# Kernel tuning notes

Hardware: AMD Instinct MI355X
Metric: run time of the kernel (lower is better)

## Reference

```python
import jax, jax.numpy as jnp
import numpy as np


def _lc2d(x, W, b, kh, kw):
    """Locally connected conv: distinct (Cout,Cin,kh,kw) kernel per output location.
    x: [B,Cin,H,W]; W: [Hout,Wout,Cout,Cin,kh,kw]; b: [Hout,Wout,Cout].
    Kernel size == stride, so each output pixel sees a disjoint kh x kw patch."""
    B, C, H, Wd = x.shape
    Hout, Wout = H // kh, Wd // kw
    patches = x.reshape(B, C, Hout, kh, Wout, kw)  # [b,c,i,k,j,l]
    out = jnp.einsum('bcikjl,ijockl->boij', patches, W)
    return out + b.transpose(2, 0, 1)[None]  # [B,Cout,Hout,Wout]


def setup_inputs() -> dict:
    key = jax.random.key(0)
    ks = jax.random.split(key, 11)

    def u(k, shape, fan_in):
        bound = 1.0 / np.sqrt(fan_in)
        return jax.random.uniform(k, shape, jnp.float32, -bound, bound)

    B = 4096
    x = jax.random.normal(ks[0], (B, 6, 60, 60), jnp.float32)
    info = jax.random.normal(ks[1], (B, 2), jnp.float32)
    # b0: 20x20 locations, Conv2d(6->32, 3x3)
    W0 = u(ks[2], (20, 20, 32, 6, 3, 3), 6 * 9)
    B0 = u(ks[3], (20, 20, 32), 6 * 9)
    # b1: 10x10 locations, Conv2d(32->64, 2x2)
    W1 = u(ks[4], (10, 10, 64, 32, 2, 2), 32 * 4)
    B1 = u(ks[5], (10, 10, 64), 32 * 4)
    # b2: 2x2 locations, Conv2d(64->128, 5x5)
    W2 = u(ks[6], (2, 2, 128, 64, 5, 5), 64 * 25)
    B2 = u(ks[7], (2, 2, 128), 64 * 25)
    # classifier Linear(514, 2); stored as [in, out]
    Wc = u(ks[8], (514, 2), 514)
    bc = u(ks[9], (2,), 514)
    return {"x": x, "info": info, "W0": W0, "B0": B0, "W1": W1, "B1": B1,
            "W2": W2, "B2": B2, "Wc": Wc, "bc": bc}


def reference(x, info, W0, B0, W1, B1, W2, B2, Wc, bc):
    h = jnp.tanh(_lc2d(x, W0, B0, 3, 3))   # [B,32,20,20]
    h = jnp.tanh(_lc2d(h, W1, B1, 2, 2))   # [B,64,10,10]
    h = jnp.tanh(_lc2d(h, W2, B2, 5, 5))   # [B,128,2,2]
    h = h.reshape(h.shape[0], -1)          # [B,512]
    h = jnp.concatenate([h, info], axis=1)  # [B,514]
    logits = h @ Wc + bc                    # [B,2]
    return jax.nn.softmax(logits, axis=1)
```

## Files before the change

kernel.cpp:

```cpp
#include <hip/hip_runtime.h>

typedef short short8 __attribute__((ext_vector_type(8)));
typedef float floatx4 __attribute__((ext_vector_type(4)));

__device__ __forceinline__ unsigned short f2bf(float f) {
  union { float f; unsigned int i; } v; v.f = f;
  return (unsigned short)((v.i + 0x7fffu + ((v.i >> 16) & 1u)) >> 16);
}
__device__ __forceinline__ float ftanh(float x) {
  float e = __expf(2.f * x);
  return 1.f - 2.f / (e + 1.f);
}

__global__ __launch_bounds__(256) void k_permute(const float* __restrict__ W0,
                                                 const float* __restrict__ W1,
                                                 const float* __restrict__ W2,
                                                 unsigned short* __restrict__ W0f,
                                                 unsigned short* __restrict__ W1f,
                                                 unsigned short* __restrict__ W2f) {
  int idx = blockIdx.x * 256 + threadIdx.x;
  int sec = idx / 819200;
  int q = idx - sec * 819200;
  int frag = q >> 9, li = q & 511;
  int lane = li >> 3, e = li & 7;
  int n = lane & 15, quad = lane >> 4;
  if (sec == 0) {
    int loc = frag >> 2, nt = (frag >> 1) & 1, ks = frag & 1;
    int kk = (ks << 5) + (quad << 3) + e;
    int co = (nt << 4) + n;
    unsigned short v = 0;
    if (kk < 54) v = f2bf(W0[loc * 1728 + co * 54 + kk]);
    W0f[q] = v;
  } else if (sec == 1) {
    int loc = frag >> 4, nt = (frag >> 2) & 3, ks = frag & 3;
    int kk = (ks << 5) + (quad << 3) + e;
    int kl = kk >> 5, c = kk & 31, co = (nt << 4) + n;
    W1f[q] = f2bf(W1[(size_t)loc * 8192 + (co << 7) + (c << 2) + kl]);
  } else {
    int g = frag / 50, ks = frag - g * 50;
    int loc = g >> 3, nt = g & 7;
    int kk = (ks << 5) + (quad << 3) + e;
    int kl5 = kk >> 6, c = kk & 63, co = (nt << 4) + n;
    W2f[q] = f2bf(W2[(size_t)loc * 204800 + co * 1600 + c * 25 + kl5]);
  }
}

__global__ __launch_bounds__(256, 2) void k_fused(const float* __restrict__ x,
                                                  const short8* __restrict__ W0f,
                                                  const float* __restrict__ B0,
                                                  const short8* __restrict__ W1f,
                                                  const float* __restrict__ B1,
                                                  const short8* __restrict__ W2f,
                                                  const float* __restrict__ B2,
                                                  float* __restrict__ h2) {
  const int t = threadIdx.x, lane = t & 63, w = t >> 6;
  const int n16 = lane & 15, quad = lane >> 4;
  const int q = blockIdx.x;
  const int b0 = blockIdx.y << 4;
  const int i0 = (q >> 1) * 5, j0 = (q & 1) * 5;

  __shared__ __align__(16) unsigned short sX[16 * 264];
  __shared__ __align__(16) unsigned short sA[16 * 136];
  __shared__ __align__(16) unsigned short sH[16 * 1608];

  const floatx4 z = {0.f, 0.f, 0.f, 0.f};
  const float* xq = x + (size_t)b0 * 21600;

  if (t < 64) {
    unsigned int* d = (unsigned int*)&sX[(t >> 2) * 264 + (t & 3) * 64 + 54];
    d[0] = 0u; d[1] = 0u; d[2] = 0u; d[3] = 0u; d[4] = 0u;
  }

  auto stage = [&](int gi, int gj) {
    const float* base = xq + gi * 360 + gj * 6;
#pragma unroll
    for (int uu = 0; uu < 3; ++uu) {
      int u = t + (uu << 8);
      if (uu == 2 && t >= 64) continue;
      int b = u / 36, rem = u - b * 36;
      int c = rem / 6, rr = rem - c * 6;
      const float2* p = (const float2*)(base + (size_t)b * 21600 + c * 3600 + rr * 60);
      float2 v0 = p[0], v1 = p[1], v2 = p[2];
      int si = (rr >= 3) ? 1 : 0, r = rr - si * 3;
      unsigned short* d0 = &sX[b * 264 + (si << 1) * 64 + c * 9 + r * 3];
      d0[0]  = f2bf(v0.x); d0[1]  = f2bf(v0.y); d0[2]  = f2bf(v1.x);
      d0[64] = f2bf(v1.y); d0[65] = f2bf(v2.x); d0[66] = f2bf(v2.y);
    }
  };

  stage(i0, j0);
  __syncthreads();

  for (int li = 0; li < 25; ++li) {
    const int di = li / 5, dj = li - di * 5;
    const int gi = i0 + di, gj = j0 + dj;

    {
      const int s = w;
      const int loc0 = (2 * gi + (s >> 1)) * 20 + (2 * gj + (s & 1));
      short8 a0 = *(const short8*)&sX[n16 * 264 + s * 64 + (quad << 3)];
      short8 a1 = *(const short8*)&sX[n16 * 264 + s * 64 + 32 + (quad << 3)];
      short8 b00 = W0f[((loc0 << 2) + 0) * 64 + lane];
      short8 b01 = W0f[((loc0 << 2) + 1) * 64 + lane];
      short8 b10 = W0f[((loc0 << 2) + 2) * 64 + lane];
      short8 b11 = W0f[((loc0 << 2) + 3) * 64 + lane];
      floatx4 acc0 = z, acc1 = z;
      acc0 = __builtin_amdgcn_mfma_f32_16x16x32_bf16(a0, b00, acc0, 0, 0, 0);
      acc0 = __builtin_amdgcn_mfma_f32_16x16x32_bf16(a1, b01, acc0, 0, 0, 0);
      acc1 = __builtin_amdgcn_mfma_f32_16x16x32_bf16(a0, b10, acc1, 0, 0, 0);
      acc1 = __builtin_amdgcn_mfma_f32_16x16x32_bf16(a1, b11, acc1, 0, 0, 0);
      float bias0 = B0[loc0 * 32 + n16];
      float bias1 = B0[loc0 * 32 + 16 + n16];
#pragma unroll
      for (int reg = 0; reg < 4; ++reg) {
        unsigned short* dd = &sA[((quad << 2) + reg) * 136 + (s << 5) + n16];
        dd[0]  = f2bf(ftanh(acc0[reg] + bias0));
        dd[16] = f2bf(ftanh(acc1[reg] + bias1));
      }
    }
    __syncthreads();

    if (li < 24) {
      const int lin = li + 1;
      const int din = lin / 5, djn = lin - din * 5;
      stage(i0 + din, j0 + djn);
    }

    {
      const int loc1 = gi * 10 + gj;
      short8 a0 = *(const short8*)&sA[n16 * 136 + 0  + (quad << 3)];
      short8 a1 = *(const short8*)&sA[n16 * 136 + 32 + (quad << 3)];
      short8 a2 = *(const short8*)&sA[n16 * 136 + 64 + (quad << 3)];
      short8 a3 = *(const short8*)&sA[n16 * 136 + 96 + (quad << 3)];
      const short8* wb = W1f + (size_t)(((loc1 << 2) + w) << 2) * 64 + lane;
      floatx4 acc = z;
      acc = __builtin_amdgcn_mfma_f32_16x16x32_bf16(a0, wb[0],   acc, 0, 0, 0);
      acc = __builtin_amdgcn_mfma_f32_16x16x32_bf16(a1, wb[64],  acc, 0, 0, 0);
      acc = __builtin_amdgcn_mfma_f32_16x16x32_bf16(a2, wb[128], acc, 0, 0, 0);
      acc = __builtin_amdgcn_mfma_f32_16x16x32_bf16(a3, wb[192], acc, 0, 0, 0);
      float bias = B1[(loc1 << 6) + (w << 4) + n16];
      int col = (li << 6) + (w << 4) + n16;
#pragma unroll
      for (int reg = 0; reg < 4; ++reg)
        sH[((quad << 2) + reg) * 1608 + col] = f2bf(ftanh(acc[reg] + bias));
    }
    __syncthreads();
  }

  floatx4 acc0 = z, acc1 = z;
  const short8* wb0 = W2f + (size_t)(((q << 3) + (w << 1)) * 50) * 64 + lane;
  const short8* wb1 = wb0 + (size_t)50 * 64;
  for (int ks = 0; ks < 50; ++ks) {
    short8 a = *(const short8*)&sH[n16 * 1608 + (ks << 5) + (quad << 3)];
    acc0 = __builtin_amdgcn_mfma_f32_16x16x32_bf16(a, wb0[ks * 64], acc0, 0, 0, 0);
    acc1 = __builtin_amdgcn_mfma_f32_16x16x32_bf16(a, wb1[ks * 64], acc1, 0, 0, 0);
  }

#pragma unroll
  for (int u = 0; u < 2; ++u) {
    const floatx4& ac = u ? acc1 : acc0;
    int co = (((w << 1) + u) << 4) + n16;
    float bias = B2[(q << 7) + co];
#pragma unroll
    for (int reg = 0; reg < 4; ++reg) {
      int bb = b0 + (quad << 2) + reg;
      h2[(size_t)bb * 512 + (co << 2) + q] = ftanh(ac[reg] + bias);
    }
  }
}

__global__ __launch_bounds__(256) void k_cls(const float* __restrict__ h2,
                                             const float* __restrict__ info,
                                             const float* __restrict__ Wc,
                                             const float* __restrict__ bc,
                                             float* __restrict__ out) {
  const int l = threadIdx.x & 63;
  const int b = blockIdx.x * 4 + (threadIdx.x >> 6);
  const float* hrow = h2 + (size_t)b * 512;
  float p0 = 0.f, p1 = 0.f;
#pragma unroll
  for (int f = 0; f < 512; f += 64) {
    float h = hrow[f + l];
    p0 = fmaf(h, Wc[2 * (f + l)], p0);
    p1 = fmaf(h, Wc[2 * (f + l) + 1], p1);
  }
#pragma unroll
  for (int m = 32; m; m >>= 1) {
    p0 += __shfl_xor(p0, m, 64);
    p1 += __shfl_xor(p1, m, 64);
  }
  if (l == 0) {
    float i0 = info[2 * b], i1 = info[2 * b + 1];
    float l0 = p0 + i0 * Wc[1024] + i1 * Wc[1026] + bc[0];
    float l1 = p1 + i0 * Wc[1025] + i1 * Wc[1027] + bc[1];
    float mx = fmaxf(l0, l1);
    float e0 = __expf(l0 - mx), e1 = __expf(l1 - mx);
    float inv = 1.f / (e0 + e1);
    out[2 * b]     = e0 * inv;
    out[2 * b + 1] = e1 * inv;
  }
}

extern "C" void kernel_launch(void* const* d_in, const int* in_sizes, int n_in,
                              void* d_out, int out_size, void* d_ws, size_t ws_size,
                              hipStream_t stream) {
  const float* x    = (const float*)d_in[0];
  const float* info = (const float*)d_in[1];
  const float* W0   = (const float*)d_in[2];
  const float* B0   = (const float*)d_in[3];
  const float* W1   = (const float*)d_in[4];
  const float* B1   = (const float*)d_in[5];
  const float* W2   = (const float*)d_in[6];
  const float* B2   = (const float*)d_in[7];
  const float* Wc   = (const float*)d_in[8];
  const float* bc   = (const float*)d_in[9];
  float* out = (float*)d_out;

  char* ws = (char*)d_ws;
  float*          h2  = (float*)ws;
  unsigned short* W0f = (unsigned short*)(ws + 8388608);
  unsigned short* W1f = (unsigned short*)(ws + 10027008);
  unsigned short* W2f = (unsigned short*)(ws + 11665408);

  k_permute<<<dim3(9600),    dim3(256), 0, stream>>>(W0, W1, W2, W0f, W1f, W2f);
  k_fused  <<<dim3(4, 256),  dim3(256), 0, stream>>>(x, (const short8*)W0f, B0,
                                                     (const short8*)W1f, B1,
                                                     (const short8*)W2f, B2, h2);
  k_cls    <<<dim3(1024),    dim3(256), 0, stream>>>(h2, info, Wc, bc, out);
}
```

Measured before the change: 697.6 us.

## Split fused kernel into layer0/1 kernel and separate layer2 GEMM kernel

Replaces the single fused kernel, which looped serially over 25 layer-1 locations per block with only 1024 blocks, with two kernels. The first computes layers 0 and 1 for a half-row of locations per block (5120 blocks, higher occupancy target) and writes bf16 activations to a global buffer laid out for layer 2. The second runs the layer-2 GEMM reading that buffer with register prefetch. This exposes far more parallelism but adds a ~50MB global round-trip for the intermediate activations.

```diff
diff --git a/kernel.cpp b/kernel.cpp
--- a/kernel.cpp
+++ b/kernel.cpp
@@ -45,115 +45,122 @@
   }
 }
 
-__global__ __launch_bounds__(256, 2) void k_fused(const float* __restrict__ x,
-                                                  const short8* __restrict__ W0f,
-                                                  const float* __restrict__ B0,
-                                                  const short8* __restrict__ W1f,
-                                                  const float* __restrict__ B1,
-                                                  const short8* __restrict__ W2f,
-                                                  const float* __restrict__ B2,
-                                                  float* __restrict__ h2) {
+__global__ __launch_bounds__(256, 3) void k_l01(const float* __restrict__ x,
+                                                const short8* __restrict__ W0f,
+                                                const float* __restrict__ B0,
+                                                const short8* __restrict__ W1f,
+                                                const float* __restrict__ B1,
+                                                unsigned short* __restrict__ h1) {
+  const int t = threadIdx.x, lane = t & 63, w = t >> 6;
+  const int n16 = lane & 15, quad = lane >> 4;
+  const int gi = blockIdx.x >> 1, jh = blockIdx.x & 1;
+  const int b0 = blockIdx.y << 4;
+
+  __shared__ __align__(16) unsigned short sX[16 * 648];
+  __shared__ __align__(16) unsigned short sA[16 * 648];
+
+  if (t < 160) {
+    unsigned int* d = (unsigned int*)&sX[(t / 10) * 648 + (t % 10) * 64 + 54];
+    d[0] = 0u; d[1] = 0u; d[2] = 0u; d[3] = 0u; d[4] = 0u;
+  }
+
+  const floatx4 z = {0.f, 0.f, 0.f, 0.f};
+
+#pragma unroll
+  for (int si = 0; si < 2; ++si) {
+    __syncthreads();
+    for (int u = t; u < 288; u += 256) {
+      int b = u / 18, rem = u - b * 18;
+      int c = rem / 3, r = rem - c * 3;
+      const float* px = x + ((size_t)(b0 + b) * 6 + c) * 3600
+                          + (6 * gi + 3 * si + r) * 60 + 30 * jh;
+      unsigned short* dst = &sX[b * 648 + c * 9 + r * 3];
+#pragma unroll
+      for (int m = 0; m < 15; ++m) {
+        float2 v = *(const float2*)(px + 2 * m);
+        const int c0 = 2 * m, c1 = 2 * m + 1;
+        dst[(c0 / 3) * 64 + (c0 % 3)] = f2bf(v.x);
+        dst[(c1 / 3) * 64 + (c1 % 3)] = f2bf(v.y);
+      }
+    }
+    __syncthreads();
+#pragma unroll
+    for (int m = 0; m < 5; ++m) {
+      const int u = w + (m << 2);
+      const int jj = u >> 1, nt = u & 1;
+      const int loc0 = (2 * gi + si) * 20 + 10 * jh + jj;
+      short8 a0 = *(const short8*)&sX[n16 * 648 + jj * 64 + (quad << 3)];
+      short8 a1 = *(const short8*)&sX[n16 * 648 + jj * 64 + 32 + (quad << 3)];
+      short8 bf0 = W0f[(loc0 * 4 + nt * 2 + 0) * 64 + lane];
+      short8 bf1 = W0f[(loc0 * 4 + nt * 2 + 1) * 64 + lane];
+      floatx4 acc = z;
+      acc = __builtin_amdgcn_mfma_f32_16x16x32_bf16(a0, bf0, acc, 0, 0, 0);
+      acc = __builtin_amdgcn_mfma_f32_16x16x32_bf16(a1, bf1, acc, 0, 0, 0);
+      const float bias = B0[loc0 * 32 + nt * 16 + n16];
+      const int base = (jj >> 1) * 128 + (si * 2 + (jj & 1)) * 32 + nt * 16 + n16;
+#pragma unroll
+      for (int reg = 0; reg < 4; ++reg)
+        sA[((quad << 2) + reg) * 648 + base] = f2bf(ftanh(acc[reg] + bias));
+    }
+  }
+  __syncthreads();
+
+  const int q2 = (gi >= 5 ? 2 : 0) + jh;
+  const int di = gi - (gi >= 5 ? 5 : 0);
+#pragma unroll
+  for (int gjl = 0; gjl < 5; ++gjl) {
+    const int loc1 = gi * 10 + 5 * jh + gjl;
+    short8 a0 = *(const short8*)&sA[n16 * 648 + gjl * 128 + 0  + (quad << 3)];
+    short8 a1 = *(const short8*)&sA[n16 * 648 + gjl * 128 + 32 + (quad << 3)];
+    short8 a2 = *(const short8*)&sA[n16 * 648 + gjl * 128 + 64 + (quad << 3)];
+    short8 a3 = *(const short8*)&sA[n16 * 648 + gjl * 128 + 96 + (quad << 3)];
+    const short8* wb = W1f + (size_t)((loc1 * 4 + w) * 4) * 64 + lane;
+    floatx4 acc = z;
+    acc = __builtin_amdgcn_mfma_f32_16x16x32_bf16(a0, wb[0],   acc, 0, 0, 0);
+    acc = __builtin_amdgcn_mfma_f32_16x16x32_bf16(a1, wb[64],  acc, 0, 0, 0);
+    acc = __builtin_amdgcn_mfma_f32_16x16x32_bf16(a2, wb[128], acc, 0, 0, 0);
+    acc = __builtin_amdgcn_mfma_f32_16x16x32_bf16(a3, wb[192], acc, 0, 0, 0);
+    const float bias = B1[loc1 * 64 + w * 16 + n16];
+    const int kl5 = di * 5 + gjl;
+    unsigned short* ob = h1 + ((size_t)(q2 * 25 + kl5) * 4096) * 64 + w * 16 + n16;
+#pragma unroll
+    for (int reg = 0; reg < 4; ++reg) {
+      int bb = b0 + (quad << 2) + reg;
+      ob[(size_t)bb * 64] = f2bf(ftanh(acc[reg] + bias));
+    }
+  }
+}
+
+__global__ __launch_bounds__(256) void k_l2(const unsigned short* __restrict__ h1,
+                                            const short8* __restrict__ W2f,
+                                            const float* __restrict__ B2,
+                                            float* __restrict__ h2) {
   const int t = threadIdx.x, lane = t & 63, w = t >> 6;
   const int n16 = lane & 15, quad = lane >> 4;
   const int q = blockIdx.x;
   const int b0 = blockIdx.y << 4;
-  const int i0 = (q >> 1) * 5, j0 = (q & 1) * 5;
-
-  __shared__ __align__(16) unsigned short sX[16 * 264];
-  __shared__ __align__(16) unsigned short sA[16 * 136];
-  __shared__ __align__(16) unsigned short sH[16 * 1608];
-
   const floatx4 z = {0.f, 0.f, 0.f, 0.f};
-  const float* xq = x + (size_t)b0 * 21600;
-
-  if (t < 64) {
-    unsigned int* d = (unsigned int*)&sX[(t >> 2) * 264 + (t & 3) * 64 + 54];
-    d[0] = 0u; d[1] = 0u; d[2] = 0u; d[3] = 0u; d[4] = 0u;
-  }
-
-  auto stage = [&](int gi, int gj) {
-    const float* base = xq + gi * 360 + gj * 6;
-#pragma unroll
-    for (int uu = 0; uu < 3; ++uu) {
-      int u = t + (uu << 8);
-      if (uu == 2 && t >= 64) continue;
-      int b = u / 36, rem = u - b * 36;
-      int c = rem / 6, rr = rem - c * 6;
-      const float2* p = (const float2*)(base + (size_t)b * 21600 + c * 3600 + rr * 60);
-      float2 v0 = p[0], v1 = p[1], v2 = p[2];
-      int si = (rr >= 3) ? 1 : 0, r = rr - si * 3;
-      unsigned short* d0 = &sX[b * 264 + (si << 1) * 64 + c * 9 + r * 3];
-      d0[0]  = f2bf(v0.x); d0[1]  = f2bf(v0.y); d0[2]  = f2bf(v1.x);
-      d0[64] = f2bf(v1.y); d0[65] = f2bf(v2.x); d0[66] = f2bf(v2.y);
-    }
-  };
-
-  stage(i0, j0);
-  __syncthreads();
-
-  for (int li = 0; li < 25; ++li) {
-    const int di = li / 5, dj = li - di * 5;
-    const int gi = i0 + di, gj = j0 + dj;
-
-    {
-      const int s = w;
-      const int loc0 = (2 * gi + (s >> 1)) * 20 + (2 * gj + (s & 1));
-      short8 a0 = *(const short8*)&sX[n16 * 264 + s * 64 + (quad << 3)];
-      short8 a1 = *(const short8*)&sX[n16 * 264 + s * 64 + 32 + (quad << 3)];
-      short8 b00 = W0f[((loc0 << 2) + 0) * 64 + lane];
-      short8 b01 = W0f[((loc0 << 2) + 1) * 64 + lane];
-      short8 b10 = W0f[((loc0 << 2) + 2) * 64 + lane];
-      short8 b11 = W0f[((loc0 << 2) + 3) * 64 + lane];
-      floatx4 acc0 = z, acc1 = z;
-      acc0 = __builtin_amdgcn_mfma_f32_16x16x32_bf16(a0, b00, acc0, 0, 0, 0);
-      acc0 = __builtin_amdgcn_mfma_f32_16x16x32_bf16(a1, b01, acc0, 0, 0, 0);
-      acc1 = __builtin_amdgcn_mfma_f32_16x16x32_bf16(a0, b10, acc1, 0, 0, 0);
-      acc1 = __builtin_amdgcn_mfma_f32_16x16x32_bf16(a1, b11, acc1, 0, 0, 0);
-      float bias0 = B0[loc0 * 32 + n16];
-      float bias1 = B0[loc0 * 32 + 16 + n16];
-#pragma unroll
-      for (int reg = 0; reg < 4; ++reg) {
-        unsigned short* dd = &sA[((quad << 2) + reg) * 136 + (s << 5) + n16];
-        dd[0]  = f2bf(ftanh(acc0[reg] + bias0));
-        dd[16] = f2bf(ftanh(acc1[reg] + bias1));
-      }
-    }
-    __syncthreads();
-
-    if (li < 24) {
-      const int lin = li + 1;
-      const int din = lin / 5, djn = lin - din * 5;
-      stage(i0 + din, j0 + djn);
-    }
-
-    {
-      const int loc1 = gi * 10 + gj;
-      short8 a0 = *(const short8*)&sA[n16 * 136 + 0  + (quad << 3)];
-      short8 a1 = *(const short8*)&sA[n16 * 136 + 32 + (quad << 3)];
-      short8 a2 = *(const short8*)&sA[n16 * 136 + 64 + (quad << 3)];
-      short8 a3 = *(const short8*)&sA[n16 * 136 + 96 + (quad << 3)];
-      const short8* wb = W1f + (size_t)(((loc1 << 2) + w) << 2) * 64 + lane;
-      floatx4 acc = z;
-      acc = __builtin_amdgcn_mfma_f32_16x16x32_bf16(a0, wb[0],   acc, 0, 0, 0);
-      acc = __builtin_amdgcn_mfma_f32_16x16x32_bf16(a1, wb[64],  acc, 0, 0, 0);
-      acc = __builtin_amdgcn_mfma_f32_16x16x32_bf16(a2, wb[128], acc, 0, 0, 0);
-      acc = __builtin_amdgcn_mfma_f32_16x16x32_bf16(a3, wb[192], acc, 0, 0, 0);
-      float bias = B1[(loc1 << 6) + (w << 4) + n16];
-      int col = (li << 6) + (w << 4) + n16;
-#pragma unroll
-      for (int reg = 0; reg < 4; ++reg)
-        sH[((quad << 2) + reg) * 1608 + col] = f2bf(ftanh(acc[reg] + bias));
-    }
-    __syncthreads();
-  }
-
-  floatx4 acc0 = z, acc1 = z;
+
+  const unsigned short* Ab = h1 + ((size_t)q * 25 * 4096 + b0 + n16) * 64 + (quad << 3);
   const short8* wb0 = W2f + (size_t)(((q << 3) + (w << 1)) * 50) * 64 + lane;
   const short8* wb1 = wb0 + (size_t)50 * 64;
-  for (int ks = 0; ks < 50; ++ks) {
-    short8 a = *(const short8*)&sH[n16 * 1608 + (ks << 5) + (quad << 3)];
-    acc0 = __builtin_amdgcn_mfma_f32_16x16x32_bf16(a, wb0[ks * 64], acc0, 0, 0, 0);
-    acc1 = __builtin_amdgcn_mfma_f32_16x16x32_bf16(a, wb1[ks * 64], acc1, 0, 0, 0);
+
+  floatx4 acc0 = z, acc1 = z;
+  short8 aA = *(const short8*)&Ab[0];
+  short8 aB = *(const short8*)&Ab[32];
+  for (int kl5 = 0; kl5 < 25; ++kl5) {
+    short8 nA = aA, nB = aB;
+    if (kl5 < 24) {
+      const unsigned short* p = Ab + (size_t)(kl5 + 1) * 262144;
+      nA = *(const short8*)&p[0];
+      nB = *(const short8*)&p[32];
+    }
+    const int ks = kl5 * 2;
+    acc0 = __builtin_amdgcn_mfma_f32_16x16x32_bf16(aA, wb0[ks * 64], acc0, 0, 0, 0);
+    acc1 = __builtin_amdgcn_mfma_f32_16x16x32_bf16(aA, wb1[ks * 64], acc1, 0, 0, 0);
+    acc0 = __builtin_amdgcn_mfma_f32_16x16x32_bf16(aB, wb0[(ks + 1) * 64], acc0, 0, 0, 0);
+    acc1 = __builtin_amdgcn_mfma_f32_16x16x32_bf16(aB, wb1[(ks + 1) * 64], acc1, 0, 0, 0);
+    aA = nA; aB = nB;
   }
 
 #pragma unroll
@@ -217,14 +224,15 @@
   float* out = (float*)d_out;
 
   char* ws = (char*)d_ws;
-  float*          h2  = (float*)ws;
-  unsigned short* W0f = (unsigned short*)(ws + 8388608);
-  unsigned short* W1f = (unsigned short*)(ws + 10027008);
-  unsigned short* W2f = (unsigned short*)(ws + 11665408);
+  unsigned short* h1  = (unsigned short*)ws;
+  float*          h2  = (float*)(ws + 52428800);
+  unsigned short* W0f = (unsigned short*)(ws + 60817408);
+  unsigned short* W1f = (unsigned short*)(ws + 62455808);
+  unsigned short* W2f = (unsigned short*)(ws + 64094208);
 
   k_permute<<<dim3(9600),    dim3(256), 0, stream>>>(W0, W1, W2, W0f, W1f, W2f);
-  k_fused  <<<dim3(4, 256),  dim3(256), 0, stream>>>(x, (const short8*)W0f, B0,
-                                                     (const short8*)W1f, B1,
-                                                     (const short8*)W2f, B2, h2);
+  k_l01    <<<dim3(20, 256), dim3(256), 0, stream>>>(x, (const short8*)W0f, B0,
+                                                     (const short8*)W1f, B1, h1);
+  k_l2     <<<dim3(4, 256),  dim3(256), 0, stream>>>(h1, (const short8*)W2f, B2, h2);
   k_cls    <<<dim3(1024),    dim3(256), 0, stream>>>(h2, info, Wc, bc, out);
 }
```

After: 596.6 us. 1.17x faster.
